# Optimization experiments

Measured on AMD Instinct MI355X. Metric: run time of the kernel, lower is better.

The kernel has to match this reference:

```python
import jax, jax.numpy as jnp
import numpy as np
import math

N_HEADS = 16
HEAD_DIM = 64
ROPE_BASE = 10000.0


def _rope_tables(T, head_dim, dtype):
    inv_freq = 1.0 / (ROPE_BASE ** (jnp.arange(0, head_dim, 2, dtype=jnp.float32) / head_dim))
    t = jnp.arange(T, dtype=jnp.float32)
    freqs = jnp.outer(t, inv_freq)          # (T, head_dim/2)
    emb = jnp.concatenate([freqs, freqs], axis=-1)  # (T, head_dim)
    return jnp.cos(emb).astype(dtype), jnp.sin(emb).astype(dtype)


def _rotate_half(x):
    x1, x2 = jnp.split(x, 2, axis=-1)
    return jnp.concatenate([-x2, x1], axis=-1)


def setup_inputs() -> dict:
    key = jax.random.key(0)
    k1, k2, k3 = jax.random.split(key, 3)
    B, T, D = 2, 2048, 1024
    x = jax.random.normal(k1, (B, T, D), dtype=jnp.float32)
    W_qkv = jax.random.normal(k2, (D, 3 * D), dtype=jnp.float32) * (1.0 / math.sqrt(D))
    W_proj = jax.random.normal(k3, (D, D), dtype=jnp.float32) * (1.0 / math.sqrt(D))
    return {"x": x, "W_qkv": W_qkv, "W_proj": W_proj}


def reference(x, W_qkv, W_proj):
    B, T, C = x.shape
    H, Dh = N_HEADS, HEAD_DIM
    qkv = x @ W_qkv                                   # (B,T,3C)
    q, k, v = jnp.split(qkv, 3, axis=-1)
    # (B,T,C) -> (B,H,T,Dh)
    q = q.reshape(B, T, H, Dh).transpose(0, 2, 1, 3)
    k = k.reshape(B, T, H, Dh).transpose(0, 2, 1, 3)
    v = v.reshape(B, T, H, Dh).transpose(0, 2, 1, 3)
    cos, sin = _rope_tables(T, Dh, x.dtype)           # (T,Dh)
    q = q * cos + _rotate_half(q) * sin
    k = k * cos + _rotate_half(k) * sin
    scale = 1.0 / math.sqrt(Dh)
    att = jnp.einsum('bhqd,bhkd->bhqk', q, k) * scale
    causal = jnp.tril(jnp.ones((T, T), dtype=bool))
    att = jnp.where(causal, att, -jnp.inf)
    att = jax.nn.softmax(att, axis=-1)
    y = jnp.einsum('bhqk,bhkd->bhqd', att, v)         # (B,H,T,Dh)
    y = y.transpose(0, 2, 1, 3).reshape(B, T, C)
    return y @ W_proj
```

## Files before the change

### kernel.cpp

```cpp
#include <hip/hip_runtime.h>
#include <hip/hip_bf16.h>
#include <math.h>

typedef __bf16 bf16_t;
typedef __bf16 bf16x8 __attribute__((ext_vector_type(8)));
typedef __bf16 bf16x4 __attribute__((ext_vector_type(4)));
typedef __bf16 bf16x2 __attribute__((ext_vector_type(2)));
typedef float  f32x4  __attribute__((ext_vector_type(4)));
typedef float  f32x16 __attribute__((ext_vector_type(16)));

__device__ __forceinline__ void gload_lds16(const void* g, void* l) {
  __builtin_amdgcn_global_load_lds((const __attribute__((address_space(1))) void*)g,
                                   (__attribute__((address_space(3))) void*)l,
                                   16, 0, 0);
}

__device__ __forceinline__ unsigned pk2(float a, float b) {
  union { bf16x2 h; unsigned u; } x;
  x.h[0] = (bf16_t)a; x.h[1] = (bf16_t)b;
  return x.u;
}
__device__ __forceinline__ bf16x8 frag4(unsigned w0, unsigned w1, unsigned w2, unsigned w3) {
  union { unsigned u[4]; bf16x8 f; } x;
  x.u[0] = w0; x.u[1] = w1; x.u[2] = w2; x.u[3] = w3;
  return x.f;
}
__device__ __forceinline__ void pls(unsigned a, unsigned b, unsigned& x, unsigned& y) {
  auto rr = __builtin_amdgcn_permlane32_swap(a, b, false, false);
  x = ((unsigned*)&rr)[0];
  y = ((unsigned*)&rr)[1];
}

__global__ __launch_bounds__(256) void prep_all(const float* __restrict__ x,
                                                const float* __restrict__ Wqkv,
                                                const float* __restrict__ Wproj,
                                                bf16_t* __restrict__ xb,
                                                bf16_t* __restrict__ wqkvt,
                                                bf16_t* __restrict__ wprojt,
                                                float2* __restrict__ csT) {
  __shared__ float tile[32][33];
  int bx = blockIdx.x;
  if (bx < 4096) {
    int idx = (bx * 256 + threadIdx.x) * 4;
    float4 v = *(const float4*)(x + idx);
    bf16x4 o;
    o[0] = (bf16_t)v.x; o[1] = (bf16_t)v.y; o[2] = (bf16_t)v.z; o[3] = (bf16_t)v.w;
    *(bf16x4*)(xb + idx) = o;
  } else if (bx < 8192) {
    const float* W; bf16_t* Wt; int K, N, n0, k0;
    if (bx < 7168) {
      W = Wqkv; Wt = wqkvt; K = 1024; N = 3072;
      int b = bx - 4096; n0 = (b % 96) * 32; k0 = (b / 96) * 32;
    } else {
      W = Wproj; Wt = wprojt; K = 1024; N = 1024;
      int b = bx - 7168; n0 = (b & 31) * 32; k0 = (b >> 5) * 32;
    }
    int tx = threadIdx.x & 31, ty = threadIdx.x >> 5;
    #pragma unroll
    for (int i = 0; i < 4; ++i) {
      int k = ty + i * 8;
      tile[k][tx] = W[(size_t)(k0 + k) * N + n0 + tx];
    }
    __syncthreads();
    #pragma unroll
    for (int i = 0; i < 4; ++i) {
      int r = ty + i * 8;
      Wt[(size_t)(n0 + r) * K + k0 + tx] = (bf16_t)tile[tx][r];
    }
  } else {
    int b = bx - 8192;
    int t = b * 4 + (threadIdx.x >> 6);
    int d = threadIdx.x & 63;
    float inv = __expf(-logf(10000.f) * (float)(d & 31) * (1.f / 32.f));
    float ang = (float)t * inv;
    float2 cs; cs.x = cosf(ang); cs.y = sinf(ang);
    csT[t * 64 + d] = cs;
  }
}

template <int MODE>
__global__ __launch_bounds__(256) void gemm_bt(const bf16_t* __restrict__ A,
                                               const bf16_t* __restrict__ Bt,
                                               void* __restrict__ Cout,
                                               const float2* __restrict__ csT,
                                               bf16_t* __restrict__ Qo,
                                               bf16_t* __restrict__ Ko,
                                               bf16_t* __restrict__ Vt,
                                               int M, int N, int K) {
  const int tid = threadIdx.x;
  const int l = tid & 63, w = tid >> 6;
  const int lr = l & 15, lg = l >> 4;
  const int nwgx = gridDim.x, nwgy = gridDim.y;
  const int orig = blockIdx.y * nwgx + blockIdx.x;
  const int cpx = (nwgx * nwgy) >> 3;
  const int s_id = (orig & 7) * cpx + (orig >> 3);
  const int bx = s_id / nwgy;
  const int by = s_id % nwgy;
  const int wr = w >> 1, wc = w & 1;
  __shared__ __align__(16) bf16_t lA[128 * 64];
  __shared__ __align__(16) bf16_t lB[128 * 64];
  f32x4 acc[4][4];
  const f32x4 zf = {0.f, 0.f, 0.f, 0.f};
  #pragma unroll
  for (int m = 0; m < 4; ++m)
    #pragma unroll
    for (int n = 0; n < 4; ++n) acc[m][n] = zf;

  const int sr8 = l >> 3;
  const int sc16 = ((l & 7) * 16) ^ (sr8 << 4);
  const char* Ab = (const char*)(A + (size_t)(by * 128) * K);
  const char* Bb = (const char*)(Bt + (size_t)(bx * 128) * K);
  const size_t rowb = (size_t)K * 2;

  for (int k0 = 0; k0 < 2 * K; k0 += 128) {
    #pragma unroll
    for (int p = 0; p < 4; ++p) {
      int row = p * 32 + w * 8 + sr8;
      gload_lds16(Ab + (size_t)row * rowb + k0 + sc16, (char*)lA + p * 4096 + w * 1024);
      gload_lds16(Bb + (size_t)row * rowb + k0 + sc16, (char*)lB + p * 4096 + w * 1024);
    }
    __syncthreads();
    #pragma unroll
    for (int kk = 0; kk < 2; ++kk) {
      bf16x8 aF[4], bF[4];
      #pragma unroll
      for (int m = 0; m < 4; ++m) {
        int row = wr * 64 + m * 16 + lr;
        aF[m] = *(const bf16x8*)((const char*)lA + row * 128 +
                                 ((kk * 64 + lg * 16) ^ ((row & 7) << 4)));
      }
      #pragma unroll
      for (int n = 0; n < 4; ++n) {
        int row = wc * 64 + n * 16 + lr;
        bF[n] = *(const bf16x8*)((const char*)lB + row * 128 +
                                 ((kk * 64 + lg * 16) ^ ((row & 7) << 4)));
      }
      #pragma unroll
      for (int m = 0; m < 4; ++m)
        #pragma unroll
        for (int n = 0; n < 4; ++n)
          acc[m][n] = __builtin_amdgcn_mfma_f32_16x16x32_bf16(aF[m], bF[n], acc[m][n], 0, 0, 0);
    }
    __syncthreads();
  }

  const int orow0 = by * 128 + wr * 64;
  if (MODE == 0) {
    const int ocol0 = bx * 128 + wc * 64;
    float* C = (float*)Cout;
    #pragma unroll
    for (int m = 0; m < 4; ++m)
      #pragma unroll
      for (int n = 0; n < 4; ++n)
        #pragma unroll
        for (int r = 0; r < 4; ++r)
          C[(size_t)(orow0 + m * 16 + lg * 4 + r) * N + ocol0 + n * 16 + lr] =
              acc[m][n][r];
  } else {
    const int region = bx >> 3;
    const int h = ((bx & 7) << 1) + wc;
    bf16_t* dst = (region == 0) ? Qo : ((region == 1) ? Ko : Vt);
    const float qsc = (region == 0) ? 0.18033688011112042f : 1.0f;
    #pragma unroll
    for (int m = 0; m < 4; ++m)
      #pragma unroll
      for (int r = 0; r < 4; ++r) {
        int grow = orow0 + m * 16 + lg * 4 + r;
        int bb = grow >> 11, t = grow & 2047;
        bf16_t* drow = dst + (((size_t)(bb * 16 + h) * 2048 + t) << 6);
        if (region < 2) {
          #pragma unroll
          for (int n = 0; n < 4; ++n) {
            int d = n * 16 + lr;
            float2 cs = csT[t * 64 + d];
            float v = acc[m][n][r];
            float pv = acc[m][n ^ 2][r];
            float rot = (n < 2) ? -pv : pv;
            drow[d] = (bf16_t)((v * cs.x + rot * cs.y) * qsc);
          }
        } else {
          #pragma unroll
          for (int n = 0; n < 4; ++n)
            drow[n * 16 + lr] = (bf16_t)acc[m][n][r];
        }
      }
  }
}

__global__ __launch_bounds__(256) void prep_vt(const bf16_t* __restrict__ Vtmp,
                                               bf16_t* __restrict__ VT) {
  int bh = blockIdx.x & 31;
  int t0 = (blockIdx.x >> 5) * 64;
  __shared__ __align__(16) bf16_t tile[64][72];
  int r = threadIdx.x >> 2, c4 = threadIdx.x & 3;
  const bf16_t* src = Vtmp + ((size_t)bh * 2048 + t0 + r) * 64 + c4 * 16;
  *(bf16x8*)&tile[r][c4 * 16] = *(const bf16x8*)src;
  *(bf16x8*)&tile[r][c4 * 16 + 8] = *(const bf16x8*)(src + 8);
  __syncthreads();
  bf16x8 v0, v1;
  #pragma unroll
  for (int i = 0; i < 8; ++i) v0[i] = tile[c4 * 16 + i][r];
  #pragma unroll
  for (int i = 0; i < 8; ++i) v1[i] = tile[c4 * 16 + 8 + i][r];
  bf16_t* dst = VT + ((size_t)bh * 64 + r) * 2048 + t0 + c4 * 16;
  *(bf16x8*)dst = v0;
  *(bf16x8*)(dst + 8) = v1;
}

__global__ __launch_bounds__(512, 4) void attn(const bf16_t* __restrict__ Q,
                                               const bf16_t* __restrict__ K,
                                               const bf16_t* __restrict__ VT,
                                               bf16_t* __restrict__ Y) {
  const int L = blockIdx.x;
  const int bh = L & 31;
  const int idx = (L & 255) >> 5;
  const int qi = (L >= 256) ? (15 - 2 * idx) : (2 * idx);
  const int b = bh >> 4, h = bh & 15;
  const int tid = threadIdx.x, l = tid & 63, w = tid >> 6;
  const int qw = w & 3, half = w >> 2;
  const int tid2 = tid & 255;
  const int l31 = l & 31, hi = l >> 5;
  const int hi4 = hi * 4, hi8 = hi * 8;
  const int qbase = qi * 128 + qw * 32;
  const int qown = qbase + l31;
  const int ntile = qi + 1;
  const int t0 = half * ntile, tend = t0 + ntile;
  const int tdiag = qbase >> 6;

  __shared__ __align__(16) char smem[65536];
  char* Kbase = smem + half * 16384;
  char* Vbase = smem + 32768 + half * 16384;

  const bf16_t* Qb = Q + (size_t)bh * 2048 * 64;
  const bf16_t* Kb0 = K + (size_t)bh * 2048 * 64;
  const bf16_t* Vb = VT + (size_t)bh * 64 * 2048;

  bf16x8 qf[4];
  #pragma unroll
  for (int kk = 0; kk < 4; ++kk)
    qf[kk] = *(const bf16x8*)(Qb + (size_t)qown * 64 + kk * 16 + hi8);

  const int srow = tid2 >> 3;
  const int scolb = (tid2 & 7) * 16;
  const int rA = srow, rB = 32 + srow;
  const int swA = scolb ^ ((rA & 7) << 4);
  const int swB = scolb ^ ((rB & 7) << 4);
  const char* KgA = (const char*)Kb0 + (size_t)t0 * 8192 + (size_t)rA * 128 + swA;
  const char* KgB = (const char*)Kb0 + (size_t)t0 * 8192 + (size_t)rB * 128 + swB;
  const char* VgA = (const char*)Vb + (size_t)t0 * 128 + (size_t)rA * 4096 + swA;
  const char* VgB = (const char*)Vb + (size_t)t0 * 128 + (size_t)rB * 4096 + swB;

  f32x16 oa[2];
  #pragma unroll
  for (int dt = 0; dt < 2; ++dt)
    #pragma unroll
    for (int r = 0; r < 16; ++r) oa[dt][r] = 0.f;
  float lacc0 = 0.f, lacc1 = 0.f;

  gload_lds16(KgA, Kbase + tid2 * 16);
  gload_lds16(KgB, Kbase + 4096 + tid2 * 16);
  gload_lds16(VgA, Vbase + tid2 * 16);
  gload_lds16(VgB, Vbase + 4096 + tid2 * 16);
  KgA += 8192; KgB += 8192; VgA += 128; VgB += 128;
  __syncthreads();

  int cur = 0;
  for (int t = t0; t < tend; ++t) {
    if (t + 1 < tend) {
      char* dK = Kbase + (cur ^ 1) * 8192;
      char* dV = Vbase + (cur ^ 1) * 8192;
      gload_lds16(KgA, dK + tid2 * 16);
      gload_lds16(KgB, dK + 4096 + tid2 * 16);
      gload_lds16(VgA, dV + tid2 * 16);
      gload_lds16(VgB, dV + 4096 + tid2 * 16);
      KgA += 8192; KgB += 8192; VgA += 128; VgB += 128;
    }
    const char* KlH = Kbase + cur * 8192;
    const char* VlH = Vbase + cur * 8192;

    if (t <= tdiag) {
      f32x16 s[2];
      #pragma unroll
      for (int sb = 0; sb < 2; ++sb)
        #pragma unroll
        for (int r = 0; r < 16; ++r) s[sb][r] = 0.f;
      __builtin_amdgcn_s_setprio(1);
      #pragma unroll
      for (int sb = 0; sb < 2; ++sb) {
        int row = sb * 32 + l31;
        const char* kr = KlH + row * 128;
        int sw = (row & 7) << 4;
        #pragma unroll
        for (int kk = 0; kk < 4; ++kk) {
          bf16x8 kf = *(const bf16x8*)(kr + ((kk * 32 + hi * 16) ^ sw));
          s[sb] = __builtin_amdgcn_mfma_f32_32x32x16_bf16(kf, qf[kk], s[sb], 0, 0, 0);
        }
      }
      __builtin_amdgcn_s_setprio(0);

      if (t == tdiag) {
        #pragma unroll
        for (int sb = 0; sb < 2; ++sb)
          #pragma unroll
          for (int r = 0; r < 16; ++r) {
            int kv = t * 64 + sb * 32 + (r & 3) + 8 * (r >> 2) + hi4;
            if (kv > qown) s[sb][r] = -__builtin_inff();
          }
      }

      #pragma unroll
      for (int r = 0; r < 16; ++r) {
        float p0 = exp2f(s[0][r]);
        float p1 = exp2f(s[1][r]);
        s[0][r] = p0; lacc0 += p0;
        s[1][r] = p1; lacc1 += p1;
      }

      #pragma unroll
      for (int sb = 0; sb < 2; ++sb) {
        unsigned a0 = pk2(s[sb][0], s[sb][1]),   a1 = pk2(s[sb][2], s[sb][3]);
        unsigned b0 = pk2(s[sb][4], s[sb][5]),   b1 = pk2(s[sb][6], s[sb][7]);
        unsigned c0 = pk2(s[sb][8], s[sb][9]),   c1 = pk2(s[sb][10], s[sb][11]);
        unsigned d0 = pk2(s[sb][12], s[sb][13]), d1 = pk2(s[sb][14], s[sb][15]);
        unsigned r0x, r0y, r1x, r1y, r2x, r2y, r3x, r3y;
        pls(a0, b0, r0x, r0y);
        pls(a1, b1, r1x, r1y);
        pls(c0, d0, r2x, r2y);
        pls(c1, d1, r3x, r3y);
        bf16x8 pf0 = frag4(r0x, r1x, r0y, r1y);
        bf16x8 pf1 = frag4(r2x, r3x, r2y, r3y);
        __builtin_amdgcn_s_setprio(1);
        #pragma unroll
        for (int kk = 0; kk < 2; ++kk) {
          bf16x8 pf = kk ? pf1 : pf0;
          #pragma unroll
          for (int dt = 0; dt < 2; ++dt) {
            int vrow = dt * 32 + l31;
            const char* vr = VlH + vrow * 128;
            bf16x8 vf = *(const bf16x8*)(vr + ((sb * 64 + kk * 32 + hi * 16) ^ ((vrow & 7) << 4)));
            oa[dt] = __builtin_amdgcn_mfma_f32_32x32x16_bf16(vf, pf, oa[dt], 0, 0, 0);
          }
        }
        __builtin_amdgcn_s_setprio(0);
      }
    }

    __syncthreads();
    cur ^= 1;
  }

  float lacc = lacc0 + lacc1;
  lacc += __shfl_xor(lacc, 32);
  float* OLDS = (float*)smem;
  float* LLDS = (float*)(smem + 32768);
  if (half == 1) {
    #pragma unroll
    for (int r = 0; r < 32; ++r)
      OLDS[r * 256 + qw * 64 + l] = oa[r >> 4][r & 15];
    LLDS[qw * 64 + l] = lacc;
  }
  __syncthreads();
  if (half == 0) {
    #pragma unroll
    for (int r = 0; r < 32; ++r)
      oa[r >> 4][r & 15] += OLDS[r * 256 + qw * 64 + l];
    float inv = 1.f / (lacc + LLDS[qw * 64 + l]);
    bf16_t* Yb = Y + (size_t)b * 2048 * 1024 + (size_t)qown * 1024 + h * 64;
    #pragma unroll
    for (int dt = 0; dt < 2; ++dt)
      #pragma unroll
      for (int g = 0; g < 4; ++g) {
        bf16x4 v;
        #pragma unroll
        for (int jj = 0; jj < 4; ++jj) v[jj] = (bf16_t)(oa[dt][g * 4 + jj] * inv);
        *(bf16x4*)(Yb + dt * 32 + g * 8 + hi4) = v;
      }
  }
}

extern "C" void kernel_launch(void* const* d_in, const int* in_sizes, int n_in,
                              void* d_out, int out_size, void* d_ws, size_t ws_size,
                              hipStream_t stream) {
  const float* x = (const float*)d_in[0];
  const float* Wqkv = (const float*)d_in[1];
  const float* Wproj = (const float*)d_in[2];
  float* out = (float*)d_out;
  char* ws = (char*)d_ws;

  bf16_t* xb     = (bf16_t*)(ws + (0u));
  bf16_t* wqkvt  = (bf16_t*)(ws + (8u << 20));
  bf16_t* wprojt = (bf16_t*)(ws + (14u << 20));
  bf16_t* Vtmp   = (bf16_t*)(ws + (16u << 20));
  bf16_t* Q      = (bf16_t*)(ws + (40u << 20));
  bf16_t* Kr     = (bf16_t*)(ws + (48u << 20));
  bf16_t* VT     = (bf16_t*)(ws + (56u << 20));
  bf16_t* Y      = (bf16_t*)(ws + (64u << 20));
  float2* csT    = (float2*)(ws + (72u << 20));

  prep_all<<<dim3(8704), dim3(256), 0, stream>>>(x, Wqkv, Wproj, xb, wqkvt, wprojt, csT);
  gemm_bt<1><<<dim3(24, 32), dim3(256), 0, stream>>>(xb, wqkvt, nullptr, csT, Q, Kr, Vtmp,
                                                     4096, 3072, 1024);
  prep_vt<<<dim3(1024), dim3(256), 0, stream>>>(Vtmp, VT);
  attn<<<dim3(512), dim3(512), 0, stream>>>(Q, Kr, VT, Y);
  gemm_bt<0><<<dim3(8, 32), dim3(256), 0, stream>>>(Y, wprojt, (void*)out, nullptr,
                                                    nullptr, nullptr, nullptr,
                                                    4096, 1024, 1024);
}
```

Before: 112.5 us.

## Split attention blocks into 64-row query tiles with 256 threads and single-buffered LDS

The attention kernel now launches 1024 blocks of 256 threads, each covering a 64-row query tile instead of 128. Each block is still split into two halves that take disjoint KV ranges, and the 32 q-tile indices are interleaved across launch slots to balance causal work. Double-buffered K/V prefetch is replaced with load-then-sync per tile, and LDS use drops to 32KB. This raises block count and occupancy and balances work better, but removes load/compute overlap within a block. It also gives up the reuse of each K/V tile across 128 query rows.

New measurement: 117.0 us. 1.04x slower.

```diff
diff --git a/kernel.cpp b/kernel.cpp
--- a/kernel.cpp
+++ b/kernel.cpp
@@ -207,29 +207,32 @@
   *(bf16x8*)(dst + 8) = v1;
 }
 
-__global__ __launch_bounds__(512, 4) void attn(const bf16_t* __restrict__ Q,
+__global__ __launch_bounds__(256, 4) void attn(const bf16_t* __restrict__ Q,
                                                const bf16_t* __restrict__ K,
                                                const bf16_t* __restrict__ VT,
                                                bf16_t* __restrict__ Y) {
   const int L = blockIdx.x;
   const int bh = L & 31;
-  const int idx = (L & 255) >> 5;
-  const int qi = (L >= 256) ? (15 - 2 * idx) : (2 * idx);
+  const int p = (L >> 5) & 7;
+  const int s = L >> 8;
+  const int j = (s == 0) ? p : (s == 1) ? (15 - p) : (s == 2) ? (16 + p) : (31 - p);
+  const int qi = j >> 1, qh = j & 1;
   const int b = bh >> 4, h = bh & 15;
   const int tid = threadIdx.x, l = tid & 63, w = tid >> 6;
-  const int qw = w & 3, half = w >> 2;
-  const int tid2 = tid & 255;
+  const int qw = w & 1, half = w >> 1;
   const int l31 = l & 31, hi = l >> 5;
   const int hi4 = hi * 4, hi8 = hi * 8;
-  const int qbase = qi * 128 + qw * 32;
+  const int qbase = qi * 128 + qh * 64 + qw * 32;
   const int qown = qbase + l31;
-  const int ntile = qi + 1;
-  const int t0 = half * ntile, tend = t0 + ntile;
-  const int tdiag = qbase >> 6;
-
-  __shared__ __align__(16) char smem[65536];
-  char* Kbase = smem + half * 16384;
-  char* Vbase = smem + 32768 + half * 16384;
+  const int tdiag = 2 * qi + qh;
+  const int ntile = tdiag + 1;
+  const int nt0 = (ntile + 1) >> 1;
+  const int tstart = half ? nt0 : 0;
+  const int myEnd = half ? ntile : nt0;
+
+  __shared__ __align__(16) char smem[32768];
+  char* Kh = smem + half * 8192;
+  char* Vh = smem + 16384 + half * 8192;
 
   const bf16_t* Qb = Q + (size_t)bh * 2048 * 64;
   const bf16_t* Kb0 = K + (size_t)bh * 2048 * 64;
@@ -240,15 +243,13 @@
   for (int kk = 0; kk < 4; ++kk)
     qf[kk] = *(const bf16x8*)(Qb + (size_t)qown * 64 + kk * 16 + hi8);
 
-  const int srow = tid2 >> 3;
-  const int scolb = (tid2 & 7) * 16;
-  const int rA = srow, rB = 32 + srow;
-  const int swA = scolb ^ ((rA & 7) << 4);
-  const int swB = scolb ^ ((rB & 7) << 4);
-  const char* KgA = (const char*)Kb0 + (size_t)t0 * 8192 + (size_t)rA * 128 + swA;
-  const char* KgB = (const char*)Kb0 + (size_t)t0 * 8192 + (size_t)rB * 128 + swB;
-  const char* VgA = (const char*)Vb + (size_t)t0 * 128 + (size_t)rA * 4096 + swA;
-  const char* VgB = (const char*)Vb + (size_t)t0 * 128 + (size_t)rB * 4096 + swB;
+  const int r8_ = l >> 3;
+  const size_t kOff = (size_t)(qw * 32 + r8_) * 128 + ((((l & 7) ^ r8_) << 4));
+  const size_t vOff = (size_t)(qw * 32 + r8_) * 4096 + ((((l & 7) ^ r8_) << 4));
+  const char* Kg = (const char*)Kb0 + (size_t)tstart * 8192 + kOff;
+  const char* Vg = (const char*)Vb + (size_t)tstart * 128 + vOff;
+  char* dK = Kh + qw * 4096 + l * 16;
+  char* dV = Vh + qw * 4096 + l * 16;
 
   f32x16 oa[2];
   #pragma unroll
@@ -257,71 +258,63 @@
     for (int r = 0; r < 16; ++r) oa[dt][r] = 0.f;
   float lacc0 = 0.f, lacc1 = 0.f;
 
-  gload_lds16(KgA, Kbase + tid2 * 16);
-  gload_lds16(KgB, Kbase + 4096 + tid2 * 16);
-  gload_lds16(VgA, Vbase + tid2 * 16);
-  gload_lds16(VgB, Vbase + 4096 + tid2 * 16);
-  KgA += 8192; KgB += 8192; VgA += 128; VgB += 128;
-  __syncthreads();
-
-  int cur = 0;
-  for (int t = t0; t < tend; ++t) {
-    if (t + 1 < tend) {
-      char* dK = Kbase + (cur ^ 1) * 8192;
-      char* dV = Vbase + (cur ^ 1) * 8192;
-      gload_lds16(KgA, dK + tid2 * 16);
-      gload_lds16(KgB, dK + 4096 + tid2 * 16);
-      gload_lds16(VgA, dV + tid2 * 16);
-      gload_lds16(VgB, dV + 4096 + tid2 * 16);
-      KgA += 8192; KgB += 8192; VgA += 128; VgB += 128;
-    }
-    const char* KlH = Kbase + cur * 8192;
-    const char* VlH = Vbase + cur * 8192;
-
-    if (t <= tdiag) {
-      f32x16 s[2];
+  for (int i = 0; i < nt0; ++i) {
+    const int myt = tstart + i;
+    const bool valid = myt < myEnd;
+    if (valid) {
+      #pragma unroll
+      for (int c = 0; c < 4; ++c) {
+        gload_lds16(Kg + c * 1024, dK + c * 1024);
+        gload_lds16(Vg + (size_t)c * 32768, dV + c * 1024);
+      }
+    }
+    Kg += 8192; Vg += 128;
+    __syncthreads();
+
+    if (valid) {
+      f32x16 sv[2];
       #pragma unroll
       for (int sb = 0; sb < 2; ++sb)
         #pragma unroll
-        for (int r = 0; r < 16; ++r) s[sb][r] = 0.f;
+        for (int r = 0; r < 16; ++r) sv[sb][r] = 0.f;
       __builtin_amdgcn_s_setprio(1);
       #pragma unroll
       for (int sb = 0; sb < 2; ++sb) {
         int row = sb * 32 + l31;
-        const char* kr = KlH + row * 128;
+        const char* kr = Kh + row * 128;
         int sw = (row & 7) << 4;
         #pragma unroll
         for (int kk = 0; kk < 4; ++kk) {
           bf16x8 kf = *(const bf16x8*)(kr + ((kk * 32 + hi * 16) ^ sw));
-          s[sb] = __builtin_amdgcn_mfma_f32_32x32x16_bf16(kf, qf[kk], s[sb], 0, 0, 0);
+          sv[sb] = __builtin_amdgcn_mfma_f32_32x32x16_bf16(kf, qf[kk], sv[sb], 0, 0, 0);
         }
       }
       __builtin_amdgcn_s_setprio(0);
 
-      if (t == tdiag) {
+      if (myt == tdiag) {
         #pragma unroll
         for (int sb = 0; sb < 2; ++sb)
           #pragma unroll
           for (int r = 0; r < 16; ++r) {
-            int kv = t * 64 + sb * 32 + (r & 3) + 8 * (r >> 2) + hi4;
-            if (kv > qown) s[sb][r] = -__builtin_inff();
+            int kv = myt * 64 + sb * 32 + (r & 3) + 8 * (r >> 2) + hi4;
+            if (kv > qown) sv[sb][r] = -__builtin_inff();
           }
       }
 
       #pragma unroll
       for (int r = 0; r < 16; ++r) {
-        float p0 = exp2f(s[0][r]);
-        float p1 = exp2f(s[1][r]);
-        s[0][r] = p0; lacc0 += p0;
-        s[1][r] = p1; lacc1 += p1;
+        float p0 = exp2f(sv[0][r]);
+        float p1 = exp2f(sv[1][r]);
+        sv[0][r] = p0; lacc0 += p0;
+        sv[1][r] = p1; lacc1 += p1;
       }
 
       #pragma unroll
       for (int sb = 0; sb < 2; ++sb) {
-        unsigned a0 = pk2(s[sb][0], s[sb][1]),   a1 = pk2(s[sb][2], s[sb][3]);
-        unsigned b0 = pk2(s[sb][4], s[sb][5]),   b1 = pk2(s[sb][6], s[sb][7]);
-        unsigned c0 = pk2(s[sb][8], s[sb][9]),   c1 = pk2(s[sb][10], s[sb][11]);
-        unsigned d0 = pk2(s[sb][12], s[sb][13]), d1 = pk2(s[sb][14], s[sb][15]);
+        unsigned a0 = pk2(sv[sb][0], sv[sb][1]),   a1 = pk2(sv[sb][2], sv[sb][3]);
+        unsigned b0 = pk2(sv[sb][4], sv[sb][5]),   b1 = pk2(sv[sb][6], sv[sb][7]);
+        unsigned c0 = pk2(sv[sb][8], sv[sb][9]),   c1 = pk2(sv[sb][10], sv[sb][11]);
+        unsigned d0 = pk2(sv[sb][12], sv[sb][13]), d1 = pk2(sv[sb][14], sv[sb][15]);
         unsigned r0x, r0y, r1x, r1y, r2x, r2y, r3x, r3y;
         pls(a0, b0, r0x, r0y);
         pls(a1, b1, r1x, r1y);
@@ -336,7 +329,7 @@
           #pragma unroll
           for (int dt = 0; dt < 2; ++dt) {
             int vrow = dt * 32 + l31;
-            const char* vr = VlH + vrow * 128;
+            const char* vr = Vh + vrow * 128;
             bf16x8 vf = *(const bf16x8*)(vr + ((sb * 64 + kk * 32 + hi * 16) ^ ((vrow & 7) << 4)));
             oa[dt] = __builtin_amdgcn_mfma_f32_32x32x16_bf16(vf, pf, oa[dt], 0, 0, 0);
           }
@@ -346,24 +339,23 @@
     }
 
     __syncthreads();
-    cur ^= 1;
   }
 
   float lacc = lacc0 + lacc1;
   lacc += __shfl_xor(lacc, 32);
   float* OLDS = (float*)smem;
-  float* LLDS = (float*)(smem + 32768);
+  float* LLDS = (float*)(smem + 16384);
   if (half == 1) {
     #pragma unroll
     for (int r = 0; r < 32; ++r)
-      OLDS[r * 256 + qw * 64 + l] = oa[r >> 4][r & 15];
+      OLDS[r * 128 + qw * 64 + l] = oa[r >> 4][r & 15];
     LLDS[qw * 64 + l] = lacc;
   }
   __syncthreads();
   if (half == 0) {
     #pragma unroll
     for (int r = 0; r < 32; ++r)
-      oa[r >> 4][r & 15] += OLDS[r * 256 + qw * 64 + l];
+      oa[r >> 4][r & 15] += OLDS[r * 128 + qw * 64 + l];
     float inv = 1.f / (lacc + LLDS[qw * 64 + l]);
     bf16_t* Yb = Y + (size_t)b * 2048 * 1024 + (size_t)qown * 1024 + h * 64;
     #pragma unroll
@@ -401,7 +393,7 @@
   gemm_bt<1><<<dim3(24, 32), dim3(256), 0, stream>>>(xb, wqkvt, nullptr, csT, Q, Kr, Vtmp,
                                                      4096, 3072, 1024);
   prep_vt<<<dim3(1024), dim3(256), 0, stream>>>(Vtmp, VT);
-  attn<<<dim3(512), dim3(512), 0, stream>>>(Q, Kr, VT, Y);
+  attn<<<dim3(1024), dim3(256), 0, stream>>>(Q, Kr, VT, Y);
   gemm_bt<0><<<dim3(8, 32), dim3(256), 0, stream>>>(Y, wprojt, (void*)out, nullptr,
                                                     nullptr, nullptr, nullptr,
                                                     4096, 1024, 1024);
```
